# Performance work log

Hardware: AMD Instinct MI355X
Metric: run time of the kernel (lower is better)

## Reference

```python
import jax, jax.numpy as jnp
import numpy as np

EPS = 1e-08


def setup_inputs() -> dict:
    key = jax.random.key(0)
    k1, k2, k3 = jax.random.split(key, 3)
    B, C, D, H, W = 2, 4, 128, 192, 192
    net_output = jax.random.normal(k1, (B, C, D, H, W), dtype=jnp.float32)
    target = jax.random.randint(k2, (B, 1, D, H, W), 0, C, dtype=jnp.int64)
    dist = jax.random.uniform(k3, (B, D, H, W), dtype=jnp.float32)
    return {"net_output": net_output, "target": target, "dist": dist}


def reference(net_output, target, dist):
    # net_output: [B, C, D, H, W]; target: [B, 1, D, H, W] int; dist: [B, D, H, W]
    B, C = net_output.shape[0], net_output.shape[1]
    # one-hot scatter along channel dim (scatter_(1, target, 1))
    cls = jnp.arange(C, dtype=target.dtype).reshape((1, C) + (1,) * (net_output.ndim - 2))
    y_onehot = (target == cls).astype(net_output.dtype)  # [B, C, D, H, W]

    # channels i >= 1: overlay dist, then per-(b, i)-slice min-max normalize
    z = y_onehot[:, 1:] * dist[:, None]  # [B, C-1, D, H, W]
    spatial_axes = tuple(range(2, z.ndim))
    mn = jnp.min(z, axis=spatial_axes, keepdims=True)
    mx = jnp.max(z, axis=spatial_axes, keepdims=True)
    zn = (z - mn) / (mx + EPS - mn)
    dist_y = jnp.concatenate([y_onehot[:, :1], zn], axis=1)  # [B, C, D, H, W]
    dist_y = jax.lax.stop_gradient(dist_y)  # built under no_grad / from non-grad leaves

    # CrossEntropyLoss with soft (probability) targets: mean over batch+spatial
    logp = jax.nn.log_softmax(net_output, axis=1)
    loss = -(dist_y * logp).sum(axis=1).mean()
    return loss
```

## Files before the change

kernel.cpp:

```cpp
#include <hip/hip_runtime.h>

#define NB 2
#define NC 4
#define NS (128 * 192 * 192)
#define NTOT (NB * NS)
#define NSQ (NS / 4)
#define EPSF 1e-8f
#define INF_BITS 0x7F800000u

struct Ws {
    unsigned int mn[6];
    unsigned int mx[6];
    unsigned int pad[4];
    double P[6];
    double Q[6];
    double R0[2];
};

__global__ void k_init(Ws* ws) {
    const int t = threadIdx.x;
    if (t < 6) {
        ws->mn[t] = INF_BITS;
        ws->mx[t] = 0u;
        ws->P[t] = 0.0;
        ws->Q[t] = 0.0;
    }
    if (t < 2) ws->R0[t] = 0.0;
}

__global__ void k_fused(const float* __restrict__ x,
                        const int* __restrict__ tgt,
                        const float* __restrict__ dist,
                        Ws* __restrict__ ws) {
    const int half = gridDim.x >> 1;
    const int b = (blockIdx.x >= half) ? 1 : 0;
    const int bid = blockIdx.x - b * half;
    const int stride = half * blockDim.x;

    const int4* t4 = (const int4*)tgt + (size_t)b * NSQ;
    const float4* d4 = (const float4*)dist + (size_t)b * NSQ;
    const float4* xb = (const float4*)x + (size_t)b * NC * NSQ;

    float mn1 = __uint_as_float(INF_BITS), mn2 = mn1, mn3 = mn1;
    float mx1 = 0.f, mx2 = 0.f, mx3 = 0.f;
    float P1 = 0.f, P2 = 0.f, P3 = 0.f;
    float Q1 = 0.f, Q2 = 0.f, Q3 = 0.f;
    float R0 = 0.f;

    for (int q = bid * blockDim.x + threadIdx.x; q < NSQ; q += stride) {
        float4 x0 = xb[q];
        float4 x1 = xb[q + NSQ];
        float4 x2 = xb[q + 2 * NSQ];
        float4 x3 = xb[q + 3 * NSQ];
        int4 t = t4[q];
        float4 d = d4[q];
        int tk[4] = {t.x, t.y, t.z, t.w};
        float dk[4] = {d.x, d.y, d.z, d.w};
#pragma unroll
        for (int k = 0; k < 4; k++) {
            float a0 = ((const float*)&x0)[k];
            float a1 = ((const float*)&x1)[k];
            float a2 = ((const float*)&x2)[k];
            float a3 = ((const float*)&x3)[k];
            float m = fmaxf(fmaxf(a0, a1), fmaxf(a2, a3));
            float e = __expf(a0 - m) + __expf(a1 - m) + __expf(a2 - m) + __expf(a3 - m);
            float lse = m + __logf(e);
            int tt = tk[k];
            float z1 = (tt == 1) ? dk[k] : 0.f;
            float z2 = (tt == 2) ? dk[k] : 0.f;
            float z3 = (tt == 3) ? dk[k] : 0.f;
            mn1 = fminf(mn1, z1); mx1 = fmaxf(mx1, z1);
            mn2 = fminf(mn2, z2); mx2 = fmaxf(mx2, z2);
            mn3 = fminf(mn3, z3); mx3 = fmaxf(mx3, z3);
            float l1 = a1 - lse, l2 = a2 - lse, l3 = a3 - lse;
            P1 += z1 * l1; P2 += z2 * l2; P3 += z3 * l3;
            Q1 += l1; Q2 += l2; Q3 += l3;
            R0 += (tt == 0) ? (a0 - lse) : 0.f;
        }
    }

    for (int off = 32; off; off >>= 1) {
        mn1 = fminf(mn1, __shfl_down(mn1, off, 64));
        mn2 = fminf(mn2, __shfl_down(mn2, off, 64));
        mn3 = fminf(mn3, __shfl_down(mn3, off, 64));
        mx1 = fmaxf(mx1, __shfl_down(mx1, off, 64));
        mx2 = fmaxf(mx2, __shfl_down(mx2, off, 64));
        mx3 = fmaxf(mx3, __shfl_down(mx3, off, 64));
        P1 += __shfl_down(P1, off, 64);
        P2 += __shfl_down(P2, off, 64);
        P3 += __shfl_down(P3, off, 64);
        Q1 += __shfl_down(Q1, off, 64);
        Q2 += __shfl_down(Q2, off, 64);
        Q3 += __shfl_down(Q3, off, 64);
        R0 += __shfl_down(R0, off, 64);
    }

    __shared__ float sv[4][13];
    const int wid = threadIdx.x >> 6;
    if ((threadIdx.x & 63) == 0) {
        sv[wid][0] = mn1; sv[wid][1] = mn2; sv[wid][2] = mn3;
        sv[wid][3] = mx1; sv[wid][4] = mx2; sv[wid][5] = mx3;
        sv[wid][6] = P1;  sv[wid][7] = P2;  sv[wid][8] = P3;
        sv[wid][9] = Q1;  sv[wid][10] = Q2; sv[wid][11] = Q3;
        sv[wid][12] = R0;
    }
    __syncthreads();
    const int i = threadIdx.x;
    if (i < 13) {
        float v = sv[0][i];
        if (i < 3)      { v = fminf(fminf(v, sv[1][i]), fminf(sv[2][i], sv[3][i])); }
        else if (i < 6) { v = fmaxf(fmaxf(v, sv[1][i]), fmaxf(sv[2][i], sv[3][i])); }
        else            { v = v + sv[1][i] + sv[2][i] + sv[3][i]; }
        if (i < 3)       atomicMin(&ws->mn[b * 3 + i], __float_as_uint(v));
        else if (i < 6)  atomicMax(&ws->mx[b * 3 + (i - 3)], __float_as_uint(v));
        else if (i < 9)  atomicAdd(&ws->P[b * 3 + (i - 6)], (double)v);
        else if (i < 12) atomicAdd(&ws->Q[b * 3 + (i - 9)], (double)v);
        else             atomicAdd(&ws->R0[b], (double)v);
    }
}

__global__ void k_final(const Ws* __restrict__ ws, float* __restrict__ out) {
    if (threadIdx.x == 0 && blockIdx.x == 0) {
        double acc = ws->R0[0] + ws->R0[1];
#pragma unroll
        for (int i = 0; i < 6; i++) {
            float mnf = __uint_as_float(ws->mn[i]);
            float mxf = __uint_as_float(ws->mx[i]);
            float sf = 1.0f / (mxf + EPSF - mnf);
            acc += (double)sf * (ws->P[i] - (double)mnf * ws->Q[i]);
        }
        out[0] = (float)(-acc / (double)NTOT);
    }
}

extern "C" void kernel_launch(void* const* d_in, const int* in_sizes, int n_in,
                              void* d_out, int out_size, void* d_ws, size_t ws_size,
                              hipStream_t stream) {
    const float* net = (const float*)d_in[0];
    const int* tgt = (const int*)d_in[1];
    const float* dist = (const float*)d_in[2];
    Ws* ws = (Ws*)d_ws;

    k_init<<<1, 64, 0, stream>>>(ws);
    k_fused<<<2304, 256, 0, stream>>>(net, tgt, dist, ws);
    k_final<<<1, 64, 0, stream>>>(ws, (float*)d_out);
}
```

Before: 280.6 us.

## Prefetch next tile in registers and replace atomics with per-block partials

The main loop now uses a compile-time trip count and double-buffers its loads in registers, fetching the next iteration's six vectors before computing the current one, so memory latency overlaps with the softmax math. Global double-precision atomics are replaced by per-block partial results written to the workspace and reduced by a 256-thread final kernel. This drops the init kernel launch. It costs extra registers per thread, which could cut occupancy despite the launch bounds hint.

```diff
diff --git a/kernel.cpp b/kernel.cpp
--- a/kernel.cpp
+++ b/kernel.cpp
@@ -8,38 +8,26 @@
 #define EPSF 1e-8f
 #define INF_BITS 0x7F800000u
 
-struct Ws {
-    unsigned int mn[6];
-    unsigned int mx[6];
-    unsigned int pad[4];
-    double P[6];
-    double Q[6];
-    double R0[2];
-};
+#define BLOCKS 2304
+#define TPB 256
+#define HALF (BLOCKS / 2)
+#define STRIDE (HALF * TPB)
+#define ITERS (NSQ / STRIDE)
 
-__global__ void k_init(Ws* ws) {
-    const int t = threadIdx.x;
-    if (t < 6) {
-        ws->mn[t] = INF_BITS;
-        ws->mx[t] = 0u;
-        ws->P[t] = 0.0;
-        ws->Q[t] = 0.0;
-    }
-    if (t < 2) ws->R0[t] = 0.0;
-}
 
-__global__ void k_fused(const float* __restrict__ x,
-                        const int* __restrict__ tgt,
-                        const float* __restrict__ dist,
-                        Ws* __restrict__ ws) {
-    const int half = gridDim.x >> 1;
-    const int b = (blockIdx.x >= half) ? 1 : 0;
-    const int bid = blockIdx.x - b * half;
-    const int stride = half * blockDim.x;
+__global__ __launch_bounds__(TPB, 4)
+void k_fused(const float* __restrict__ x,
+             const int* __restrict__ tgt,
+             const float* __restrict__ dist,
+             float* __restrict__ part) {
+    const int b = (blockIdx.x >= HALF) ? 1 : 0;
+    const int bid = blockIdx.x - b * HALF;
 
     const int4* t4 = (const int4*)tgt + (size_t)b * NSQ;
     const float4* d4 = (const float4*)dist + (size_t)b * NSQ;
     const float4* xb = (const float4*)x + (size_t)b * NC * NSQ;
+
+    const int q0 = bid * TPB + threadIdx.x;
 
     float mn1 = __uint_as_float(INF_BITS), mn2 = mn1, mn3 = mn1;
     float mx1 = 0.f, mx2 = 0.f, mx3 = 0.f;
@@ -47,35 +35,48 @@
     float Q1 = 0.f, Q2 = 0.f, Q3 = 0.f;
     float R0 = 0.f;
 
-    for (int q = bid * blockDim.x + threadIdx.x; q < NSQ; q += stride) {
-        float4 x0 = xb[q];
-        float4 x1 = xb[q + NSQ];
-        float4 x2 = xb[q + 2 * NSQ];
-        float4 x3 = xb[q + 3 * NSQ];
-        int4 t = t4[q];
-        float4 d = d4[q];
-        int tk[4] = {t.x, t.y, t.z, t.w};
-        float dk[4] = {d.x, d.y, d.z, d.w};
+    auto vox = [&](float a0, float a1, float a2, float a3, int tt, float dv) {
+        float m = fmaxf(fmaxf(a0, a1), fmaxf(a2, a3));
+        float e = __expf(a0 - m) + __expf(a1 - m) + __expf(a2 - m) + __expf(a3 - m);
+        float lse = m + __logf(e);
+        float z1 = (tt == 1) ? dv : 0.f;
+        float z2 = (tt == 2) ? dv : 0.f;
+        float z3 = (tt == 3) ? dv : 0.f;
+        mn1 = fminf(mn1, z1); mx1 = fmaxf(mx1, z1);
+        mn2 = fminf(mn2, z2); mx2 = fmaxf(mx2, z2);
+        mn3 = fminf(mn3, z3); mx3 = fmaxf(mx3, z3);
+        float l1 = a1 - lse, l2 = a2 - lse, l3 = a3 - lse;
+        P1 += z1 * l1; P2 += z2 * l2; P3 += z3 * l3;
+        Q1 += l1; Q2 += l2; Q3 += l3;
+        R0 += (tt == 0) ? (a0 - lse) : 0.f;
+    };
+
+    float4 cx0 = xb[q0];
+    float4 cx1 = xb[q0 + NSQ];
+    float4 cx2 = xb[q0 + 2 * NSQ];
+    float4 cx3 = xb[q0 + 3 * NSQ];
+    int4 ct = t4[q0];
+    float4 cd = d4[q0];
+
 #pragma unroll
-        for (int k = 0; k < 4; k++) {
-            float a0 = ((const float*)&x0)[k];
-            float a1 = ((const float*)&x1)[k];
-            float a2 = ((const float*)&x2)[k];
-            float a3 = ((const float*)&x3)[k];
-            float m = fmaxf(fmaxf(a0, a1), fmaxf(a2, a3));
-            float e = __expf(a0 - m) + __expf(a1 - m) + __expf(a2 - m) + __expf(a3 - m);
-            float lse = m + __logf(e);
-            int tt = tk[k];
-            float z1 = (tt == 1) ? dk[k] : 0.f;
-            float z2 = (tt == 2) ? dk[k] : 0.f;
-            float z3 = (tt == 3) ? dk[k] : 0.f;
-            mn1 = fminf(mn1, z1); mx1 = fmaxf(mx1, z1);
-            mn2 = fminf(mn2, z2); mx2 = fmaxf(mx2, z2);
-            mn3 = fminf(mn3, z3); mx3 = fmaxf(mx3, z3);
-            float l1 = a1 - lse, l2 = a2 - lse, l3 = a3 - lse;
-            P1 += z1 * l1; P2 += z2 * l2; P3 += z3 * l3;
-            Q1 += l1; Q2 += l2; Q3 += l3;
-            R0 += (tt == 0) ? (a0 - lse) : 0.f;
+    for (int i = 0; i < ITERS; i++) {
+        float4 nx0, nx1, nx2, nx3, nd;
+        int4 nt;
+        if (i + 1 < ITERS) {
+            const int qn = q0 + (i + 1) * STRIDE;
+            nx0 = xb[qn];
+            nx1 = xb[qn + NSQ];
+            nx2 = xb[qn + 2 * NSQ];
+            nx3 = xb[qn + 3 * NSQ];
+            nt = t4[qn];
+            nd = d4[qn];
+        }
+        vox(cx0.x, cx1.x, cx2.x, cx3.x, ct.x, cd.x);
+        vox(cx0.y, cx1.y, cx2.y, cx3.y, ct.y, cd.y);
+        vox(cx0.z, cx1.z, cx2.z, cx3.z, ct.z, cd.z);
+        vox(cx0.w, cx1.w, cx2.w, cx3.w, ct.w, cd.w);
+        if (i + 1 < ITERS) {
+            cx0 = nx0; cx1 = nx1; cx2 = nx2; cx3 = nx3; ct = nt; cd = nd;
         }
     }
 
@@ -108,26 +109,71 @@
     const int i = threadIdx.x;
     if (i < 13) {
         float v = sv[0][i];
-        if (i < 3)      { v = fminf(fminf(v, sv[1][i]), fminf(sv[2][i], sv[3][i])); }
-        else if (i < 6) { v = fmaxf(fmaxf(v, sv[1][i]), fmaxf(sv[2][i], sv[3][i])); }
-        else            { v = v + sv[1][i] + sv[2][i] + sv[3][i]; }
-        if (i < 3)       atomicMin(&ws->mn[b * 3 + i], __float_as_uint(v));
-        else if (i < 6)  atomicMax(&ws->mx[b * 3 + (i - 3)], __float_as_uint(v));
-        else if (i < 9)  atomicAdd(&ws->P[b * 3 + (i - 6)], (double)v);
-        else if (i < 12) atomicAdd(&ws->Q[b * 3 + (i - 9)], (double)v);
-        else             atomicAdd(&ws->R0[b], (double)v);
+        if (i < 3)      v = fminf(fminf(v, sv[1][i]), fminf(sv[2][i], sv[3][i]));
+        else if (i < 6) v = fmaxf(fmaxf(v, sv[1][i]), fmaxf(sv[2][i], sv[3][i]));
+        else            v = v + sv[1][i] + sv[2][i] + sv[3][i];
+        part[(size_t)blockIdx.x * 16 + i] = v;
     }
 }
 
-__global__ void k_final(const Ws* __restrict__ ws, float* __restrict__ out) {
-    if (threadIdx.x == 0 && blockIdx.x == 0) {
-        double acc = ws->R0[0] + ws->R0[1];
+__global__ __launch_bounds__(256, 1)
+void k_final(const float* __restrict__ part, float* __restrict__ out) {
+    const int t = threadIdx.x;
+    const int batch = t >> 7;
+    const int lane7 = t & 127;
+
+    float mn[3] = {__uint_as_float(INF_BITS), __uint_as_float(INF_BITS), __uint_as_float(INF_BITS)};
+    float mx[3] = {0.f, 0.f, 0.f};
+    double P[3] = {0, 0, 0}, Q[3] = {0, 0, 0}, R0 = 0;
+
+    for (int k = 0; k < HALF / 128; k++) {
+        const float* r = part + (size_t)(batch * HALF + k * 128 + lane7) * 16;
 #pragma unroll
-        for (int i = 0; i < 6; i++) {
-            float mnf = __uint_as_float(ws->mn[i]);
-            float mxf = __uint_as_float(ws->mx[i]);
-            float sf = 1.0f / (mxf + EPSF - mnf);
-            acc += (double)sf * (ws->P[i] - (double)mnf * ws->Q[i]);
+        for (int j = 0; j < 3; j++) {
+            mn[j] = fminf(mn[j], r[j]);
+            mx[j] = fmaxf(mx[j], r[3 + j]);
+            P[j] += (double)r[6 + j];
+            Q[j] += (double)r[9 + j];
+        }
+        R0 += (double)r[12];
+    }
+
+    for (int off = 32; off; off >>= 1) {
+#pragma unroll
+        for (int j = 0; j < 3; j++) {
+            mn[j] = fminf(mn[j], __shfl_down(mn[j], off, 64));
+            mx[j] = fmaxf(mx[j], __shfl_down(mx[j], off, 64));
+            P[j] += __shfl_down(P[j], off, 64);
+            Q[j] += __shfl_down(Q[j], off, 64);
+        }
+        R0 += __shfl_down(R0, off, 64);
+    }
+
+    __shared__ float smn[4][3], smx[4][3];
+    __shared__ double sP[4][3], sQ[4][3], sR[4];
+    const int wid = t >> 6;
+    if ((t & 63) == 0) {
+#pragma unroll
+        for (int j = 0; j < 3; j++) {
+            smn[wid][j] = mn[j]; smx[wid][j] = mx[j];
+            sP[wid][j] = P[j];   sQ[wid][j] = Q[j];
+        }
+        sR[wid] = R0;
+    }
+    __syncthreads();
+    if (t == 0) {
+        double acc = 0.0;
+#pragma unroll
+        for (int b = 0; b < 2; b++) {
+            const int w0 = 2 * b, w1 = 2 * b + 1;
+            acc += sR[w0] + sR[w1];
+#pragma unroll
+            for (int j = 0; j < 3; j++) {
+                float mnf = fminf(smn[w0][j], smn[w1][j]);
+                float mxf = fmaxf(smx[w0][j], smx[w1][j]);
+                float sf = 1.0f / (mxf + EPSF - mnf);
+                acc += (double)sf * ((sP[w0][j] + sP[w1][j]) - (double)mnf * (sQ[w0][j] + sQ[w1][j]));
+            }
         }
         out[0] = (float)(-acc / (double)NTOT);
     }
@@ -139,9 +185,8 @@
     const float* net = (const float*)d_in[0];
     const int* tgt = (const int*)d_in[1];
     const float* dist = (const float*)d_in[2];
-    Ws* ws = (Ws*)d_ws;
+    float* part = (float*)d_ws;
 
-    k_init<<<1, 64, 0, stream>>>(ws);
-    k_fused<<<2304, 256, 0, stream>>>(net, tgt, dist, ws);
-    k_final<<<1, 64, 0, stream>>>(ws, (float*)d_out);
+    k_fused<<<BLOCKS, TPB, 0, stream>>>(net, tgt, dist, part);
+    k_final<<<1, 256, 0, stream>>>(part, (float*)d_out);
 }
```

Measured after the change: 281.0 us. About the same (+0.1%).
